# Kernel tuning notes

Hardware: AMD Instinct MI355X
Metric: run time of the kernel (lower is better)

## Reference

```python
import jax, jax.numpy as jnp
import numpy as np

N = 100_000
E = 1_600_000
D_IN, D_HID, D_OUT = 512, 256, 256


def setup_inputs() -> dict:
    key = jax.random.key(0)
    ks = jax.random.split(key, 10)
    x = jax.random.normal(ks[0], (N, D_IN), dtype=jnp.float32)
    edge_index = jax.random.randint(ks[1], (2, E), 0, N, dtype=jnp.int64)
    edge_weight = jax.random.uniform(ks[2], (E,), dtype=jnp.float32)
    # Glorot-ish init for the per-layer linear weights (PyG GCNConv: Linear w/o bias, bias added after aggregation)
    W1 = jax.random.normal(ks[3], (D_IN, D_HID), dtype=jnp.float32) * (1.0 / np.sqrt(D_IN))
    b1 = jnp.zeros((D_HID,), dtype=jnp.float32)
    W2 = jax.random.normal(ks[4], (D_HID, D_HID), dtype=jnp.float32) * (1.0 / np.sqrt(D_HID))
    b2 = jnp.zeros((D_HID,), dtype=jnp.float32)
    W3 = jax.random.normal(ks[5], (D_HID, D_OUT), dtype=jnp.float32) * (1.0 / np.sqrt(D_HID))
    b3 = jnp.zeros((D_OUT,), dtype=jnp.float32)
    return {"x": x, "edge_index": edge_index, "edge_weight": edge_weight,
            "W1": W1, "b1": b1, "W2": W2, "b2": b2, "W3": W3, "b3": b3}


def gcn_layer(h_in, W, b, row, col, ew, n):
    # PyG GCNConv with normalize=True, add_self_loops=True (fill value 1.0), aggr='add':
    # h = X W; deg[i] = sum of incoming edge weights (incl. self loop);
    # norm_e = deg^-1/2[row] * w_e * deg^-1/2[col]; out[col] += norm_e * h[row]; out += bias
    h = h_in @ W                                            # [n, d_out]
    deg = jnp.zeros((n,), h.dtype).at[col].add(ew) + 1.0    # +1 from self loop
    dinv = jnp.where(deg > 0, jax.lax.rsqrt(deg), 0.0)      # deg_inv_sqrt, inf -> 0
    norm = dinv[row] * ew * dinv[col]                       # [E]
    out = jnp.zeros_like(h).at[col].add(norm[:, None] * h[row])
    out = out + (dinv * dinv)[:, None] * h                  # self-loop contribution (norm_ii = dinv_i^2)
    return out + b


def reference(x, edge_index, edge_weight, W1, b1, W2, b2, W3, b3):
    row, col = edge_index[0], edge_index[1]
    n = x.shape[0]
    # dropout p=0.0 -> identity
    h = jax.nn.relu(gcn_layer(x, W1, b1, row, col, edge_weight, n))
    h = jax.nn.relu(gcn_layer(h, W2, b2, row, col, edge_weight, n))
    return gcn_layer(h, W3, b3, row, col, edge_weight, n)
```

## Files before the change

### kernel.cpp

```cpp
#include <hip/hip_runtime.h>
#include <hip/hip_bf16.h>


#define D 256
#define ELLW 48
#define BSH2 9
#define NB2MAX 256
#define DEPTH 16
#define GCAP 8960
#define FIXSCALE 1099511627776.0f
#define FIXINV   9.094947017729282e-13

typedef unsigned short ushort_t;
typedef unsigned long long u64;
typedef float f32x2 __attribute__((ext_vector_type(2)));
typedef float f32x4 __attribute__((ext_vector_type(4)));
typedef short bf16x8 __attribute__((ext_vector_type(8)));
typedef unsigned int u32x4 __attribute__((ext_vector_type(4)));

__device__ __forceinline__ float blo(unsigned u) { return __uint_as_float(u << 16); }
__device__ __forceinline__ float bhi(unsigned u) { return __uint_as_float(u & 0xFFFF0000u); }
__device__ __forceinline__ ushort_t f2b(float f) {
    unsigned u = __float_as_uint(f);
    return (ushort_t)((u + 0x7FFFu + ((u >> 16) & 1u)) >> 16);
}
__device__ __forceinline__ void gload_lds16(const ushort_t* g, ushort_t* l) {
    __builtin_amdgcn_global_load_lds((const __attribute__((address_space(1))) unsigned int*)g,
                                     (__attribute__((address_space(3))) unsigned int*)l, 16, 0, 0);
}

__global__ void zero_gfill(int* __restrict__ gfill, int nb) {
    if ((int)threadIdx.x < nb) gfill[threadIdx.x] = 0;
}

__global__ __launch_bounds__(256) void bin_p1(const int* __restrict__ row,
                                              const int* __restrict__ col,
                                              const float* __restrict__ ew,
                                              int* __restrict__ gfill,
                                              u64* __restrict__ bins, int E, int nb) {
    __shared__ u64 lbuf[196][DEPTH];
    __shared__ int lcnt[196];
    const int t = threadIdx.x;
    if (t < 196) lcnt[t] = 0;
    __syncthreads();
    int per = (E + gridDim.x - 1) / gridDim.x;
    int e0 = blockIdx.x * per;
    int e1 = e0 + per;
    if (e1 > E) e1 = E;
    for (int base = e0; base < e1; base += 256) {
        int e = base + t;
        if (e < e1) {
            int c = __builtin_nontemporal_load(&col[e]);
            int r = __builtin_nontemporal_load(&row[e]);
            float w = __builtin_nontemporal_load(&ew[e]);
            int b = c >> BSH2;
            u64 rec = ((u64)__float_as_uint(w) << 32) | ((u64)(unsigned)r << 9) |
                      (unsigned)(c & ((1 << BSH2) - 1));
            int pos = atomicAdd(&lcnt[b], 1);
            if (pos < DEPTH) {
                lbuf[b][pos] = rec;
            } else {
                int gp = atomicAdd(&gfill[b], 1);
                if (gp < GCAP) bins[(size_t)b * GCAP + gp] = rec;
                atomicSub(&lcnt[b], 1);
            }
        }
        __syncthreads();
        if (t < nb) {
            int c = lcnt[t];
            int k8 = c & ~7;
            if (k8 > 0) {
                int gp = atomicAdd(&gfill[t], k8);
                for (int i = 0; i < k8; ++i)
                    if (gp + i < GCAP) bins[(size_t)t * GCAP + gp + i] = lbuf[t][i];
                int rem = c - k8;
                for (int i = 0; i < rem; ++i) lbuf[t][i] = lbuf[t][k8 + i];
                lcnt[t] = rem;
            }
        }
        __syncthreads();
    }
    if (t < nb) {
        int c = lcnt[t];
        if (c > 0) {
            int gp = atomicAdd(&gfill[t], c);
            for (int i = 0; i < c; ++i)
                if (gp + i < GCAP) bins[(size_t)t * GCAP + gp + i] = lbuf[t][i];
        }
    }
}

__global__ __launch_bounds__(256) void bin_p2(const u64* __restrict__ bins,
                                              const int* __restrict__ gfill,
                                              int* __restrict__ cnt,
                                              float* __restrict__ dinv,
                                              u64* __restrict__ ell, int N) {
    __shared__ u64 sacc[1 << BSH2];
    const int b = blockIdx.x, t = threadIdx.x;
    const int base = b << BSH2;
    for (int i = t; i < (1 << BSH2); i += 256) sacc[i] = 0ull;
    __syncthreads();
    int fill = gfill[b];
    if (fill > GCAP) fill = GCAP;
    for (int i = t; i < fill; i += 256) {
        u64 rec = bins[(size_t)b * GCAP + i];
        int li = (int)(rec & ((1 << BSH2) - 1));
        unsigned r = (unsigned)((rec >> 9) & 0x1FFFFu);
        unsigned wb = (unsigned)(rec >> 32);
        u64 pack = (1ull << 48) | (u64)(__uint_as_float(wb) * FIXSCALE);
        int pos = (int)(atomicAdd(&sacc[li], pack) >> 48);
        if (pos < ELLW)
            ell[(size_t)(base + li) * ELLW + pos] = ((u64)wb << 32) | r;
    }
    __syncthreads();
    for (int i = t; i < (1 << BSH2); i += 256) {
        int node = base + i;
        if (node < N) {
            u64 p = sacc[i];
            int m = (int)(p >> 48);
            cnt[node] = (m > ELLW) ? ELLW : m;
            float sum = (float)((double)(p & 0xFFFFFFFFFFFFull) * FIXINV);
            dinv[node] = rsqrtf(sum + 1.0f);
        }
    }
}

__global__ __launch_bounds__(256) void cvtT_kernel(const float* __restrict__ W,
                                                   ushort_t* __restrict__ WT, int K, int C) {
    int i = blockIdx.x * 256 + threadIdx.x;
    if (i < K * C) {
        int c = i / K, k = i - c * K;
        WT[i] = f2b(W[(size_t)k * C + c]);
    }
}

template <int K, bool AF32>
__global__ __launch_bounds__(256) void gemm_mfma(const void* __restrict__ Ap,
                                                 const ushort_t* __restrict__ WT,
                                                 ushort_t* __restrict__ C, int nvalid) {
    __shared__ ushort_t As[128 * 64];
    __shared__ ushort_t Bs[256 * 64];
    const int tid = threadIdx.x;
    const int lane = tid & 63, wave = tid >> 6;
    const int wrow = wave >> 1, wcol = wave & 1;
    const int fr = lane & 15, fq = lane >> 4;
    const int r0 = blockIdx.x * 128;

    f32x4 acc[4][8] = {};

    for (int k0 = 0; k0 < K; k0 += 64) {
        if constexpr (AF32) {
            const float* Af = (const float*)Ap;
#pragma unroll
            for (int i = 0; i < 8; ++i) {
                int idx = i * 256 + tid;
                int rowt = idx >> 4;
                int c4 = idx & 15;
                int grow = r0 + rowt;
                if (grow >= nvalid) grow = nvalid - 1;
                f32x4 v = __builtin_nontemporal_load(
                    (const f32x4*)&Af[(size_t)grow * K + k0 + c4 * 4]);
                __hip_bfloat162 b01 = __float22bfloat162_rn(make_float2(v[0], v[1]));
                __hip_bfloat162 b23 = __float22bfloat162_rn(make_float2(v[2], v[3]));
                uint2 st = make_uint2(*(unsigned*)&b01, *(unsigned*)&b23);
                int slot = c4 >> 1, half = c4 & 1;
                int off = rowt * 64 + ((slot ^ (rowt & 7)) << 3) + (half << 2);
                *(uint2*)&As[off] = st;
            }
        } else {
            const ushort_t* Ab = (const ushort_t*)Ap;
#pragma unroll
            for (int q = 0; q < 4; ++q) {
                int qa = wave * 4 + q;
                int rowt = qa * 8 + (lane >> 3);
                int g = (lane & 7) ^ (lane >> 3);
                gload_lds16(&Ab[(size_t)(r0 + rowt) * K + k0 + g * 8], &As[qa * 512]);
            }
        }
#pragma unroll
        for (int q = 0; q < 8; ++q) {
            int qb = wave * 8 + q;
            int rowt = qb * 8 + (lane >> 3);
            int g = (lane & 7) ^ (lane >> 3);
            gload_lds16(&WT[(size_t)rowt * K + k0 + g * 8], &Bs[qb * 512]);
        }
        __syncthreads();

#pragma unroll
        for (int kk = 0; kk < 2; ++kk) {
            int g = (kk * 4 + fq) ^ (fr & 7);
            bf16x8 aF[4];
#pragma unroll
            for (int m = 0; m < 4; ++m) {
                int arow = wrow * 64 + m * 16 + fr;
                aF[m] = *(const bf16x8*)&As[arow * 64 + g * 8];
            }
#pragma unroll
            for (int n = 0; n < 8; ++n) {
                int bcol = wcol * 128 + n * 16 + fr;
                bf16x8 bF = *(const bf16x8*)&Bs[bcol * 64 + g * 8];
#pragma unroll
                for (int m = 0; m < 4; ++m)
                    acc[m][n] = __builtin_amdgcn_mfma_f32_16x16x32_bf16(
                        bF, aF[m], acc[m][n], 0, 0, 0);
            }
        }
        __syncthreads();
    }

#pragma unroll
    for (int m = 0; m < 4; ++m) {
        int gr = r0 + wrow * 64 + m * 16 + fr;
        if (gr < nvalid) {
#pragma unroll
            for (int n = 0; n < 8; ++n) {
                ushort4 h;
                h.x = f2b(acc[m][n][0]); h.y = f2b(acc[m][n][1]);
                h.z = f2b(acc[m][n][2]); h.w = f2b(acc[m][n][3]);
                *(ushort4*)&C[(size_t)gr * D + wcol * 128 + n * 16 + fq * 4] = h;
            }
        }
    }
}

template <bool RELU, bool OUTF32>
__global__ __launch_bounds__(256) void agg_half(const ushort_t* __restrict__ hb,
                                                const float* __restrict__ dinv,
                                                const float* __restrict__ bias,
                                                const int* __restrict__ cnt,
                                                const u64* __restrict__ ell,
                                                void* __restrict__ outp, int N, int fb) {
    int node = blockIdx.x * 4 + (threadIdx.x >> 6);
    if (node >= N) return;
    int lane = threadIdx.x & 63;
    int q = lane >> 4;
    int fl = lane & 15;
    float dn = dinv[node], d2 = dn * dn;

    u32x4 sv = *(const u32x4*)&hb[(size_t)node * 256 + fb + fl * 8];
    float sc = (q == 0) ? d2 : 0.f;
    float a[8];
#pragma unroll
    for (int i = 0; i < 4; ++i) { a[2 * i] = sc * blo(sv[i]); a[2 * i + 1] = sc * bhi(sv[i]); }

    int m = cnt[node];
    int srcl = 0;
    float wl = 0.f;
    if (lane < m) {
        u64 r = __builtin_nontemporal_load(&ell[(size_t)node * ELLW + lane]);
        srcl = (int)(unsigned)r;
        wl = dinv[srcl] * __uint_as_float((unsigned)(r >> 32)) * dn;
    }
    int steps = (m + 3) >> 2;
#pragma unroll 2
    for (int j = 0; j < steps; ++j) {
        int idx = 4 * j + q;
        int src = __shfl(srcl, idx);
        float w = __shfl(wl, idx);
        u32x4 v = *(const u32x4*)&hb[(size_t)src * 256 + fb + fl * 8];
#pragma unroll
        for (int i = 0; i < 4; ++i) {
            a[2 * i]     = fmaf(w, blo(v[i]), a[2 * i]);
            a[2 * i + 1] = fmaf(w, bhi(v[i]), a[2 * i + 1]);
        }
    }
#pragma unroll
    for (int i = 0; i < 8; ++i) {
        a[i] += __shfl_xor(a[i], 16);
        a[i] += __shfl_xor(a[i], 32);
    }
    float r0, r1;
    if (q == 0)      { r0 = a[0]; r1 = a[1]; }
    else if (q == 1) { r0 = a[2]; r1 = a[3]; }
    else if (q == 2) { r0 = a[4]; r1 = a[5]; }
    else             { r0 = a[6]; r1 = a[7]; }
    int feat = fb + fl * 8 + q * 2;
    f32x2 bb = *(const f32x2*)&bias[feat];
    r0 += bb[0]; r1 += bb[1];
    if (RELU) { r0 = fmaxf(r0, 0.f); r1 = fmaxf(r1, 0.f); }
    if (OUTF32) {
        f32x2 o = {r0, r1};
        __builtin_nontemporal_store(o, (f32x2*)((float*)outp + (size_t)node * 256 + feat));
    } else {
        unsigned p = (unsigned)f2b(r0) | ((unsigned)f2b(r1) << 16);
        __builtin_nontemporal_store(p, (unsigned*)((ushort_t*)outp + (size_t)node * 256 + feat));
    }
}

extern "C" void kernel_launch(void* const* d_in, const int* in_sizes, int n_in,
                              void* d_out, int out_size, void* d_ws, size_t ws_size,
                              hipStream_t stream) {
    const float* x  = (const float*)d_in[0];
    const int*   ei = (const int*)d_in[1];
    const float* ew = (const float*)d_in[2];
    const float* W1 = (const float*)d_in[3];
    const float* b1 = (const float*)d_in[4];
    const float* W2 = (const float*)d_in[5];
    const float* b2 = (const float*)d_in[6];
    const float* W3 = (const float*)d_in[7];
    const float* b3 = (const float*)d_in[8];
    const int N = in_sizes[0] / 512;
    const int E = in_sizes[2];
    const int* row = ei;
    const int* col = ei + E;
    float* out = (float*)d_out;

    const int MB = (N + 127) / 128;
    const size_t Npad = (size_t)MB * 128;
    const int NB2 = (N + (1 << BSH2) - 1) >> BSH2;

    char* ws = (char*)d_ws;
    size_t off = 0;
    auto alloc = [&](size_t bytes) -> void* {
        void* p = ws + off;
        off += (bytes + 255) / 256 * 256;
        return p;
    };
    ushort_t* hb  = (ushort_t*)alloc(Npad * D * sizeof(ushort_t));
    u64*      ell = (u64*)alloc((size_t)N * ELLW * sizeof(u64));
    ushort_t* WT1 = (ushort_t*)alloc((size_t)512 * D * sizeof(ushort_t));
    ushort_t* WT2 = (ushort_t*)alloc((size_t)256 * D * sizeof(ushort_t));
    ushort_t* WT3 = (ushort_t*)alloc((size_t)256 * D * sizeof(ushort_t));
    int*   cnt    = (int*)alloc((size_t)N * sizeof(int));
    float* dinv   = (float*)alloc((size_t)N * sizeof(float));
    int*   gfill  = (int*)alloc((size_t)NB2MAX * sizeof(int));
    u64*   bins   = (u64*)hb;
    ushort_t* ab  = (ushort_t*)d_out;

    int gE = (E + 255) / 256;
    int gA = (N + 3) / 4;
    zero_gfill<<<1, 256, 0, stream>>>(gfill, NB2);
    cvtT_kernel<<<(512 * D + 255) / 256, 256, 0, stream>>>(W1, WT1, 512, D);
    cvtT_kernel<<<(256 * D + 255) / 256, 256, 0, stream>>>(W2, WT2, 256, D);
    cvtT_kernel<<<(256 * D + 255) / 256, 256, 0, stream>>>(W3, WT3, 256, D);
    bin_p1<<<512, 256, 0, stream>>>(row, col, ew, gfill, bins, E, NB2);
    bin_p2<<<NB2, 256, 0, stream>>>(bins, gfill, cnt, dinv, ell, N);

    gemm_mfma<512, true><<<MB, 256, 0, stream>>>(x, WT1, hb, N);
    agg_half<true, false><<<gA, 256, 0, stream>>>(hb, dinv, b1, cnt, ell, ab, N, 0);
    agg_half<true, false><<<gA, 256, 0, stream>>>(hb, dinv, b1, cnt, ell, ab, N, 128);
    gemm_mfma<256, false><<<MB, 256, 0, stream>>>(ab, WT2, hb, N);
    agg_half<true, false><<<gA, 256, 0, stream>>>(hb, dinv, b2, cnt, ell, ab, N, 0);
    agg_half<true, false><<<gA, 256, 0, stream>>>(hb, dinv, b2, cnt, ell, ab, N, 128);
    gemm_mfma<256, false><<<MB, 256, 0, stream>>>(ab, WT3, hb, N);
    agg_half<false, true><<<gA, 256, 0, stream>>>(hb, dinv, b3, cnt, ell, out, N, 0);
    agg_half<false, true><<<gA, 256, 0, stream>>>(hb, dinv, b3, cnt, ell, out, N, 128);
}
```

Before: 752.1 us.

## Merge two half-feature aggregation passes into one full-row aggregation kernel

The aggregation previously ran twice per layer, each pass covering 128 features with four edge-groups of 16 lanes. Now one wavefront handles all 256 features: two edge-groups of 32 lanes each read a full 512-byte bf16 row. This halves kernel launches and the repeated reads of ELL indices, dinv and self rows, and makes each gather a larger contiguous load. In exchange there is less edge-level parallelism per wave and a longer dependent loop per node, with the working set per pass twice as large for the cache.

```diff
diff --git a/kernel.cpp b/kernel.cpp
--- a/kernel.cpp
+++ b/kernel.cpp
@@ -224,24 +224,25 @@
 }
 
 template <bool RELU, bool OUTF32>
-__global__ __launch_bounds__(256) void agg_half(const ushort_t* __restrict__ hb,
-                                                const float* __restrict__ dinv,
-                                                const float* __restrict__ bias,
-                                                const int* __restrict__ cnt,
-                                                const u64* __restrict__ ell,
-                                                void* __restrict__ outp, int N, int fb) {
+__global__ __launch_bounds__(256) void agg_kernel(const ushort_t* __restrict__ hb,
+                                                  const float* __restrict__ dinv,
+                                                  const float* __restrict__ bias,
+                                                  const int* __restrict__ cnt,
+                                                  const u64* __restrict__ ell,
+                                                  void* __restrict__ outp, int N) {
     int node = blockIdx.x * 4 + (threadIdx.x >> 6);
     if (node >= N) return;
     int lane = threadIdx.x & 63;
-    int q = lane >> 4;
-    int fl = lane & 15;
+    int half = lane >> 5;
+    int fl = lane & 31;
     float dn = dinv[node], d2 = dn * dn;
 
-    u32x4 sv = *(const u32x4*)&hb[(size_t)node * 256 + fb + fl * 8];
-    float sc = (q == 0) ? d2 : 0.f;
-    float a[8];
-#pragma unroll
-    for (int i = 0; i < 4; ++i) { a[2 * i] = sc * blo(sv[i]); a[2 * i + 1] = sc * bhi(sv[i]); }
+    u32x4 sv = *(const u32x4*)&hb[(size_t)node * 256 + fl * 8];
+    float sc = half ? 0.f : d2;
+    float a0 = sc * blo(sv.x), a1 = sc * bhi(sv.x);
+    float a2 = sc * blo(sv.y), a3 = sc * bhi(sv.y);
+    float a4 = sc * blo(sv.z), a5 = sc * bhi(sv.z);
+    float a6 = sc * blo(sv.w), a7 = sc * bhi(sv.w);
 
     int m = cnt[node];
     int srcl = 0;
@@ -251,39 +252,40 @@
         srcl = (int)(unsigned)r;
         wl = dinv[srcl] * __uint_as_float((unsigned)(r >> 32)) * dn;
     }
-    int steps = (m + 3) >> 2;
-#pragma unroll 2
+    int steps = (m + 1) >> 1;
+#pragma unroll 4
     for (int j = 0; j < steps; ++j) {
-        int idx = 4 * j + q;
-        int src = __shfl(srcl, idx);
-        float w = __shfl(wl, idx);
-        u32x4 v = *(const u32x4*)&hb[(size_t)src * 256 + fb + fl * 8];
-#pragma unroll
-        for (int i = 0; i < 4; ++i) {
-            a[2 * i]     = fmaf(w, blo(v[i]), a[2 * i]);
-            a[2 * i + 1] = fmaf(w, bhi(v[i]), a[2 * i + 1]);
-        }
-    }
-#pragma unroll
-    for (int i = 0; i < 8; ++i) {
-        a[i] += __shfl_xor(a[i], 16);
-        a[i] += __shfl_xor(a[i], 32);
-    }
-    float r0, r1;
-    if (q == 0)      { r0 = a[0]; r1 = a[1]; }
-    else if (q == 1) { r0 = a[2]; r1 = a[3]; }
-    else if (q == 2) { r0 = a[4]; r1 = a[5]; }
-    else             { r0 = a[6]; r1 = a[7]; }
-    int feat = fb + fl * 8 + q * 2;
-    f32x2 bb = *(const f32x2*)&bias[feat];
-    r0 += bb[0]; r1 += bb[1];
-    if (RELU) { r0 = fmaxf(r0, 0.f); r1 = fmaxf(r1, 0.f); }
+        int idx2 = 2 * j + half;
+        int src = __shfl(srcl, idx2);
+        float w = __shfl(wl, idx2);
+        u32x4 v = *(const u32x4*)&hb[(size_t)src * 256 + fl * 8];
+        a0 = fmaf(w, blo(v.x), a0); a1 = fmaf(w, bhi(v.x), a1);
+        a2 = fmaf(w, blo(v.y), a2); a3 = fmaf(w, bhi(v.y), a3);
+        a4 = fmaf(w, blo(v.z), a4); a5 = fmaf(w, bhi(v.z), a5);
+        a6 = fmaf(w, blo(v.w), a6); a7 = fmaf(w, bhi(v.w), a7);
+    }
+    a0 += __shfl_xor(a0, 32); a1 += __shfl_xor(a1, 32);
+    a2 += __shfl_xor(a2, 32); a3 += __shfl_xor(a3, 32);
+    a4 += __shfl_xor(a4, 32); a5 += __shfl_xor(a5, 32);
+    a6 += __shfl_xor(a6, 32); a7 += __shfl_xor(a7, 32);
+    float r0 = half ? a4 : a0;
+    float r1 = half ? a5 : a1;
+    float r2 = half ? a6 : a2;
+    float r3 = half ? a7 : a3;
+    f32x4 bb = *(const f32x4*)&bias[fl * 8 + half * 4];
+    r0 += bb[0]; r1 += bb[1]; r2 += bb[2]; r3 += bb[3];
+    if (RELU) {
+        r0 = fmaxf(r0, 0.f); r1 = fmaxf(r1, 0.f);
+        r2 = fmaxf(r2, 0.f); r3 = fmaxf(r3, 0.f);
+    }
     if (OUTF32) {
-        f32x2 o = {r0, r1};
-        __builtin_nontemporal_store(o, (f32x2*)((float*)outp + (size_t)node * 256 + feat));
+        f32x4 o = {r0, r1, r2, r3};
+        __builtin_nontemporal_store(
+            o, (f32x4*)((float*)outp + (size_t)node * 256 + fl * 8 + half * 4));
     } else {
-        unsigned p = (unsigned)f2b(r0) | ((unsigned)f2b(r1) << 16);
-        __builtin_nontemporal_store(p, (unsigned*)((ushort_t*)outp + (size_t)node * 256 + feat));
+        u64 p = (u64)f2b(r0) | ((u64)f2b(r1) << 16) | ((u64)f2b(r2) << 32) | ((u64)f2b(r3) << 48);
+        __builtin_nontemporal_store(
+            p, (u64*)((ushort_t*)outp + (size_t)node * 256 + fl * 8 + half * 4));
     }
 }
 
@@ -327,7 +329,6 @@
     u64*   bins   = (u64*)hb;
     ushort_t* ab  = (ushort_t*)d_out;
 
-    int gE = (E + 255) / 256;
     int gA = (N + 3) / 4;
     zero_gfill<<<1, 256, 0, stream>>>(gfill, NB2);
     cvtT_kernel<<<(512 * D + 255) / 256, 256, 0, stream>>>(W1, WT1, 512, D);
@@ -337,12 +338,9 @@
     bin_p2<<<NB2, 256, 0, stream>>>(bins, gfill, cnt, dinv, ell, N);
 
     gemm_mfma<512, true><<<MB, 256, 0, stream>>>(x, WT1, hb, N);
-    agg_half<true, false><<<gA, 256, 0, stream>>>(hb, dinv, b1, cnt, ell, ab, N, 0);
-    agg_half<true, false><<<gA, 256, 0, stream>>>(hb, dinv, b1, cnt, ell, ab, N, 128);
+    agg_kernel<true, false><<<gA, 256, 0, stream>>>(hb, dinv, b1, cnt, ell, ab, N);
     gemm_mfma<256, false><<<MB, 256, 0, stream>>>(ab, WT2, hb, N);
-    agg_half<true, false><<<gA, 256, 0, stream>>>(hb, dinv, b2, cnt, ell, ab, N, 0);
-    agg_half<true, false><<<gA, 256, 0, stream>>>(hb, dinv, b2, cnt, ell, ab, N, 128);
+    agg_kernel<true, false><<<gA, 256, 0, stream>>>(hb, dinv, b2, cnt, ell, ab, N);
     gemm_mfma<256, false><<<MB, 256, 0, stream>>>(ab, WT3, hb, N);
-    agg_half<false, true><<<gA, 256, 0, stream>>>(hb, dinv, b3, cnt, ell, out, N, 0);
-    agg_half<false, true><<<gA, 256, 0, stream>>>(hb, dinv, b3, cnt, ell, out, N, 128);
-}
+    agg_kernel<false, true><<<gA, 256, 0, stream>>>(hb, dinv, b3, cnt, ell, out, N);
+}
```

Measured after the change: 711.5 us. 5.4% less time.
